# Kernel optimization log

Measured on AMD Instinct MI355X. Metric: run time of the kernel, lower is better.

## Reference

```python
import jax, jax.numpy as jnp
import numpy as np
from jax import lax

W_MAX = 8
STEP = 1
LEAK = 2
KSIZE = (W_MAX - 1) * (STEP + LEAK)  # 21 = kernel size, padding, and fodep
THETA = 80
FODEP = KSIZE
OUT_CH = 1
NEURONS = 1024


def make_w_kernel_table():
    # StepFireLeak response table: [w_max, ksize], flipped in time
    w_idx = np.arange(W_MAX, dtype=np.float32)[:, None]
    t_idx = np.arange(KSIZE, dtype=np.float32)[None, :]
    w_step = np.maximum(np.floor(1.0 + t_idx / STEP), 0.0)
    w_leak = np.maximum(np.ceil(w_idx + ((w_idx - 1.0) * STEP - t_idx) / LEAK), 0.0)
    table = np.minimum(w_step, w_leak).astype(np.int32)[:, ::-1]
    return jnp.asarray(np.ascontiguousarray(table))


def setup_inputs() -> dict:
    key = jax.random.key(0)
    k1, k2 = jax.random.split(key)
    B, C, S, T = 64, 1, 784, 500
    input_spikes = (jax.random.uniform(k1, (B, C, S, T)) < 0.05).astype(jnp.float32)
    # integer synaptic weights in [0, w_max)
    weight = jax.random.randint(k2, (OUT_CH * NEURONS, C * S), 0, W_MAX, dtype=jnp.int32)
    return {"input_spikes": input_spikes, "weight": weight}


def reference(input_spikes, weight):
    B, C, S, T = input_spikes.shape
    x = input_spikes.reshape(B, C * S, T)
    # expand integer weights into response kernels: [out, in, ksize]
    table = make_w_kernel_table().astype(jnp.float32)
    kern = table[weight]
    pot = lax.conv_general_dilated(
        x, kern, window_strides=(1,), padding=[(KSIZE, KSIZE)],
        dimension_numbers=("NCH", "OIH", "NCH"))
    pot = jnp.rint(pot).astype(jnp.int32)
    Tp = pot.shape[-1]  # T + ksize + 1
    pot = pot.reshape(B, OUT_CH, NEURONS, Tp)
    pot_t = jnp.transpose(pot, (3, 0, 1, 2))  # [Tp, B, C, N]

    def step(dep, p):  # dep: [B, C] int32, p: [B, C, N]
        winner = jnp.argmax(p, axis=-1)  # [B, C]
        val = jnp.take_along_axis(p, winner[..., None], axis=-1)[..., 0]
        cond = ((val > THETA) & (dep == 0)).astype(jnp.int32)  # min_depression == 0
        winners_t = jax.nn.one_hot(winner, NEURONS, dtype=jnp.int32) * cond[..., None]
        new_dep = jnp.maximum(0, dep + cond * (FODEP + 1) - 1)
        return new_dep, winners_t

    dep0 = jnp.zeros((B, OUT_CH), dtype=jnp.int32)
    _, winners = lax.scan(step, dep0, pot_t)  # [Tp, B, C, N]
    return jnp.transpose(winners, (1, 2, 3, 0))  # [B, C, N, Tp]
```

## Files before the change

### kernel.cpp

```cpp
#include <hip/hip_runtime.h>

#define B_DIM 64
#define S_DIM 784
#define T_DIM 500
#define N_DIM 1024
#define TP    522
#define KS    21
#define THETA 80
#define NCHUNK 8
#define CH    66
#define LISTCAP 128
#define SW64  13
#define BMSTRIDE 16

__global__ void k_prep(const int* __restrict__ w, unsigned char* __restrict__ wt9) {
  unsigned idx = blockIdx.x * 256 + threadIdx.x;
  if (idx < S_DIM * N_DIM) {
    unsigned s = idx >> 10, n = idx & 1023;
    int wv = w[n * S_DIM + s];
    wt9[idx] = wv ? (unsigned char)(9 * (wv - 1)) : (unsigned char)63;
  }
}

__global__ void __launch_bounds__(1024)
k_bitmap(const float* __restrict__ x, unsigned long long* __restrict__ bm) {
  __shared__ unsigned long long s_m[S_DIM];
  const int tid = threadIdx.x;
  const int wave = tid >> 6, lane = tid & 63;
  const int b = blockIdx.y;
  const int t0 = blockIdx.x * 64;
  const int t = t0 + lane;
  const bool tok = (t < T_DIM);
  const float* xb = x + (size_t)b * S_DIM * T_DIM;

  for (int s = wave; s < S_DIM; s += 16) {
    float v = tok ? xb[(size_t)s * T_DIM + t] : 0.0f;
    unsigned long long m = __ballot(v != 0.0f);
    if (lane == 0) s_m[s] = m;
  }
  __syncthreads();

  if (wave < SW64) {
    const int sbase = wave * 64;
    const unsigned long long mask_s =
        (sbase + lane < S_DIM) ? s_m[sbase + lane] : 0ull;
    unsigned long long* dst = bm + ((size_t)b * 512 + t0) * BMSTRIDE + wave;
    for (int tl = 0; tl < 64; ++tl) {
      unsigned long long wrd = __ballot((mask_s >> tl) & 1ull);
      if (lane == 0) dst[(size_t)tl * BMSTRIDE] = wrd;
    }
  }
}

__global__ void __launch_bounds__(1024, 8)
k_main(const unsigned char* __restrict__ wt9,
       const unsigned long long* __restrict__ bm,
       unsigned* __restrict__ red) {
  __shared__ unsigned short s_list[87][LISTCAP];
  __shared__ int s_cnt[87];
  __shared__ unsigned smax[CH];

  const int tid = threadIdx.x;
  const int b = blockIdx.y;
  const int lo = blockIdx.x * CH;
  const int hi = min(TP - 1, lo + CH - 1);
  const int t0 = max(0, lo - KS);
  const int n_emit = hi - lo + 1;
  const int nt_in = min(hi, T_DIM - 1) - t0 + 1;

  for (int i = tid; i < nt_in; i += 1024) s_cnt[i] = 0;
  for (int i = tid; i < n_emit; i += 1024) smax[i] = 0u;
  __syncthreads();

  const unsigned long long* bmb = bm + ((size_t)b * 512 + t0) * BMSTRIDE;
  const int ntask = nt_in * SW64;
  for (int task = tid; task < ntask; task += 1024) {
    const int li = task / SW64;
    const int sw = task - li * SW64;
    unsigned long long w = bmb[(size_t)li * BMSTRIDE + sw];
    if (w) {
      int c = __popcll(w);
      int pos = atomicAdd(&s_cnt[li], c);
      const int sb = sw * 64;
      while (w) {
        int j = __builtin_ctzll(w);
        if (pos < LISTCAP) s_list[li][pos] = (unsigned short)(sb + j);
        ++pos;
        w &= (w - 1);
      }
    }
  }
  __syncthreads();

  int ring[KS + 1];
  #pragma unroll
  for (int i = 0; i <= KS; ++i) ring[i] = 0;

  const unsigned invn = (unsigned)(1023 - tid);

  for (int t = t0; t <= hi; ++t) {
    if (t >= lo) {
      unsigned key = ((unsigned)ring[0] << 10) | invn;
      #pragma unroll
      for (int off = 32; off > 0; off >>= 1) {
        unsigned o = __shfl_xor(key, off, 64);
        key = key > o ? key : o;
      }
      if ((tid & 63) == 0) atomicMax(&smax[t - lo], key);
    }

    if (t < T_DIM) {
      const int li = t - t0;
      const int cnt = __builtin_amdgcn_readfirstlane(min(s_cnt[li], LISTCAP));
      const unsigned short* lp = &s_list[li][0];
      unsigned long long ca = 0, cb = 0;
      int i = 0;
      for (; i + 1 < cnt; i += 2) {
        unsigned ia = ((unsigned)lp[i] << 10) + tid;
        unsigned ib = ((unsigned)lp[i + 1] << 10) + tid;
        ca += 1ull << wt9[ia];
        cb += 1ull << wt9[ib];
      }
      if (i < cnt) ca += 1ull << wt9[((unsigned)lp[i] << 10) + tid];
      const unsigned long long c = ca + cb;

      const int c1 = (int)(c & 511), c2 = (int)((c >> 9) & 511), c3 = (int)((c >> 18) & 511),
                c4 = (int)((c >> 27) & 511), c5 = (int)((c >> 36) & 511),
                c6 = (int)((c >> 45) & 511), c7 = (int)((c >> 54) & 511);
      const int S7 = c7, S6 = S7 + c6, S5 = S6 + c5, S4 = S5 + c4,
                S3 = S4 + c3, S2 = S3 + c2, S1 = S2 + c1;
      const int O1 = c1, O3 = O1 + c3, O5 = O3 + c5, O7 = O5 + c7;
      const int E2 = c2, E4 = E2 + c4, E6 = E4 + c6;
      const int O31 = O3 - O1, O51 = O5 - O1, O71 = O7 - O1,
                O73 = O7 - O3, O75 = O7 - O5;
      const int E62 = E6 - E2, E64 = E6 - E4;
      int acc = S1;        ring[1]  += acc;
      acc += S2;           ring[2]  += acc;
      acc += S3 - O1;      ring[3]  += acc;
      acc += S4 - E2;      ring[4]  += acc;
      acc += S5 - O31;     ring[5]  += acc;
      acc += S6 - E4;      ring[6]  += acc;
      acc += S7 - O51;     ring[7]  += acc;
      acc -= E62;          ring[8]  += acc;
      acc -= O71;          ring[9]  += acc;
      acc -= E62;          ring[10] += acc;
      acc -= O73;          ring[11] += acc;
      acc -= E62;          ring[12] += acc;
      acc -= O73;          ring[13] += acc;
      acc -= E64;          ring[14] += acc;
      acc -= O73;          ring[15] += acc;
      acc -= E64;          ring[16] += acc;
      acc -= O75;          ring[17] += acc;
      acc -= E64;          ring[18] += acc;
      acc -= O75;          ring[19] += acc;
                           ring[20] += acc;
      acc -= O75;          ring[21] += acc;
    }

    #pragma unroll
    for (int i = 0; i < KS; ++i) ring[i] = ring[i + 1];
    ring[KS] = 0;
  }

  __syncthreads();
  for (int i = tid; i < n_emit; i += 1024)
    red[(unsigned)b * TP + (unsigned)(lo + i)] = smax[i];
}

__global__ void k_scan(const unsigned* __restrict__ red, int* __restrict__ out) {
  int b = threadIdx.x;
  if (b >= B_DIM) return;
  int dep = 0;
  for (int base = 0; base < TP; base += 6) {
    unsigned buf[6];
    #pragma unroll
    for (int k = 0; k < 6; ++k) buf[k] = red[b * TP + base + k];
    #pragma unroll
    for (int k = 0; k < 6; ++k) {
      unsigned key = buf[k];
      int val = (int)(key >> 10);
      bool cond = (val > THETA) && (dep == 0);
      if (cond) {
        int idx = 1023 - (int)(key & 1023);
        out[(b * N_DIM + idx) * TP + base + k] = 1;
        dep = 22;
      }
      dep = max(0, dep - 1);
    }
  }
}

extern "C" void kernel_launch(void* const* d_in, const int* in_sizes, int n_in,
                              void* d_out, int out_size, void* d_ws, size_t ws_size,
                              hipStream_t stream) {
  const float* x = (const float*)d_in[0];
  const int* wgt = (const int*)d_in[1];
  int* out = (int*)d_out;

  unsigned char* wt9      = (unsigned char*)d_ws;
  unsigned long long* bm  = (unsigned long long*)((char*)d_ws + 802816);
  unsigned* red           = (unsigned*)((char*)d_ws + 802816 + 4194304);

  hipMemsetAsync(d_out, 0, (size_t)out_size * sizeof(int), stream);
  k_prep<<<3136, 256, 0, stream>>>(wgt, wt9);
  k_bitmap<<<dim3(8, B_DIM), 1024, 0, stream>>>(x, bm);
  k_main<<<dim3(NCHUNK, B_DIM), 1024, 0, stream>>>(wt9, bm, red);
  k_scan<<<1, 64, 0, stream>>>(red, out);
}
```

Before: 612.7 us.

## Replace output memset with fused winner-fill kernel and wave-parallel scan

Drops the full-output memset plus scattered one-writes. The sequential scan now records a per-(batch,time) winner index into a workspace buffer, using one wave per batch that loads keys with a coalesced read and broadcasts them with shuffles. A new fill kernel then writes the whole output tensor once with vectorized int2 stores, each element set by comparing against the winner. Output traffic stays about the same (one full write instead of memset plus scatters), but it saves a launch/memset pass and makes the scan's loads coalesced, at the cost of rereading the small winner array for every neuron.

```diff
diff --git a/kernel.cpp b/kernel.cpp
--- a/kernel.cpp
+++ b/kernel.cpp
@@ -167,26 +167,42 @@
     red[(unsigned)b * TP + (unsigned)(lo + i)] = smax[i];
 }
 
-__global__ void k_scan(const unsigned* __restrict__ red, int* __restrict__ out) {
-  int b = threadIdx.x;
-  if (b >= B_DIM) return;
+__global__ void __launch_bounds__(256)
+k_scan(const unsigned* __restrict__ red, unsigned* __restrict__ winner) {
+  const int wv = (int)((blockIdx.x * 256 + threadIdx.x) >> 6);
+  const int lane = threadIdx.x & 63;
+  if (wv >= B_DIM) return;
+  const unsigned* r = red + wv * TP;
+  unsigned* wn = winner + wv * TP;
   int dep = 0;
-  for (int base = 0; base < TP; base += 6) {
-    unsigned buf[6];
-    #pragma unroll
-    for (int k = 0; k < 6; ++k) buf[k] = red[b * TP + base + k];
-    #pragma unroll
-    for (int k = 0; k < 6; ++k) {
-      unsigned key = buf[k];
-      int val = (int)(key >> 10);
-      bool cond = (val > THETA) && (dep == 0);
-      if (cond) {
-        int idx = 1023 - (int)(key & 1023);
-        out[(b * N_DIM + idx) * TP + base + k] = 1;
-        dep = 22;
-      }
+  for (int base = 0; base < TP; base += 64) {
+    const int nt = min(64, TP - base);
+    unsigned key = (lane < nt) ? r[base + lane] : 0u;
+    unsigned w = 0;
+    for (int j = 0; j < nt; ++j) {
+      unsigned kj = __shfl(key, j, 64);
+      bool cond = ((int)(kj >> 10) > THETA) && (dep == 0);
+      if (cond && lane == j) w = 1024u - (kj & 1023u);
+      dep += cond ? 22 : 0;
       dep = max(0, dep - 1);
     }
+    if (lane < nt) wn[base + lane] = w;
+  }
+}
+
+__global__ void __launch_bounds__(256)
+k_fill(const unsigned* __restrict__ winner, int* __restrict__ out) {
+  const int n = blockIdx.x;
+  const int b = blockIdx.y;
+  const unsigned* wn = winner + b * TP;
+  int* o = out + ((size_t)b * N_DIM + n) * TP;
+  const unsigned target = (unsigned)(n + 1);
+  int2* o2 = (int2*)o;
+  for (int i = threadIdx.x; i < TP / 2; i += 256) {
+    int2 v;
+    v.x = (wn[2 * i]     == target) ? 1 : 0;
+    v.y = (wn[2 * i + 1] == target) ? 1 : 0;
+    o2[i] = v;
   }
 }
 
@@ -200,10 +216,11 @@
   unsigned char* wt9      = (unsigned char*)d_ws;
   unsigned long long* bm  = (unsigned long long*)((char*)d_ws + 802816);
   unsigned* red           = (unsigned*)((char*)d_ws + 802816 + 4194304);
-
-  hipMemsetAsync(d_out, 0, (size_t)out_size * sizeof(int), stream);
+  unsigned* winner        = (unsigned*)((char*)d_ws + 802816 + 4194304 + 133632);
+
   k_prep<<<3136, 256, 0, stream>>>(wgt, wt9);
   k_bitmap<<<dim3(8, B_DIM), 1024, 0, stream>>>(x, bm);
   k_main<<<dim3(NCHUNK, B_DIM), 1024, 0, stream>>>(wt9, bm, red);
-  k_scan<<<1, 64, 0, stream>>>(red, out);
-}
+  k_scan<<<(B_DIM * 64 + 255) / 256, 256, 0, stream>>>(red, winner);
+  k_fill<<<dim3(N_DIM, B_DIM), 256, 0, stream>>>(winner, out);
+}
```

Result: no change. 615.9 us (+0.5%).
